# Kernel tuning notes

Measured on AMD Instinct MI355X. Metric: run time of the kernel, lower is better.

## Reference

```python
import jax, jax.numpy as jnp
import numpy as np

N_NODES = 50000
N_EDGES = 800000
F = 128
LN_EPS = 1e-5


def _sage_conv(h, src, dst, Wl, bl, Wr, n_nodes):
    # PyG SAGEConv (aggr='mean', root_weight=True):
    #   out_i = lin_l(mean_{j->i} h_j) + lin_r(h_i)
    msg = h[src]  # [E, F] irregular gather
    s = jax.ops.segment_sum(msg, dst, num_segments=n_nodes)  # [N, F]
    deg = jax.ops.segment_sum(jnp.ones((src.shape[0],), h.dtype), dst,
                              num_segments=n_nodes)  # [N]
    mean = s / jnp.maximum(deg, 1.0)[:, None]
    return mean @ Wl.T + bl + h @ Wr.T


def _graph_layernorm(h, w, b):
    # PyG LayerNorm mode='graph', batch=None: normalize over ALL entries,
    # eps added to std, then per-channel affine.
    m = h.mean()
    std = jnp.sqrt(jnp.mean((h - m) ** 2))
    return (h - m) / (std + LN_EPS) * w + b


def _prelu(h, w):
    # nn.PReLU(1): single shared slope
    return jnp.where(h >= 0, h, w * h)


def setup_inputs() -> dict:
    key = jax.random.key(0)
    ks = jax.random.split(key, 12)
    sc = 1.0 / np.sqrt(F)
    x = jax.random.normal(ks[0], (N_NODES, F), dtype=jnp.float32)
    edge_index = jax.random.randint(ks[1], (2, N_EDGES), 0, N_NODES, dtype=jnp.int64)
    return {
        "x": x,
        "edge_index": edge_index,
        "Wl0": jax.random.uniform(ks[2], (F, F), jnp.float32, -sc, sc),
        "bl0": jnp.zeros((F,), jnp.float32),
        "Wr0": jax.random.uniform(ks[3], (F, F), jnp.float32, -sc, sc),
        "ln_w0": jnp.ones((F,), jnp.float32),
        "ln_b0": jnp.zeros((F,), jnp.float32),
        "pw0": jnp.full((1,), 0.25, jnp.float32),
        "skipW0": jax.random.uniform(ks[4], (F, F), jnp.float32, -sc, sc),
        "Wl1": jax.random.uniform(ks[5], (F, F), jnp.float32, -sc, sc),
        "bl1": jnp.zeros((F,), jnp.float32),
        "Wr1": jax.random.uniform(ks[6], (F, F), jnp.float32, -sc, sc),
        "ln_w1": jnp.ones((F,), jnp.float32),
        "ln_b1": jnp.zeros((F,), jnp.float32),
        "pw1": jnp.full((1,), 0.25, jnp.float32),
    }


def reference(x, edge_index, Wl0, bl0, Wr0, ln_w0, ln_b0, pw0, skipW0,
              Wl1, bl1, Wr1, ln_w1, ln_b1, pw1):
    src, dst = edge_index[0], edge_index[1]
    n = x.shape[0]
    # layer 0: h = x
    h = _sage_conv(x, src, dst, Wl0, bl0, Wr0, n)
    h = _graph_layernorm(h, ln_w0, ln_b0)
    h1 = _prelu(h, pw0)
    # layer 1: h = skip(x) + h1
    h = x @ skipW0.T + h1
    h = _sage_conv(h, src, dst, Wl1, bl1, Wr1, n)
    h = _graph_layernorm(h, ln_w1, ln_b1)
    h = _prelu(h, pw1)
    return h
```

## Files before the change

kernel.cpp:

```cpp
#include <hip/hip_runtime.h>

#define LN_EPS 1e-5f
#define BUCKCAP 2048
#define PCHUNK 6656
#define PK 13

typedef short bf16x8 __attribute__((ext_vector_type(8)));
typedef float f32x4  __attribute__((ext_vector_type(4)));

static __device__ __forceinline__ float4 ld4(const float* p){ return *(const float4*)p; }
static __device__ __forceinline__ uint f2bf1(float f){
  uint u = __float_as_uint(f);
  return (u + 0x7fffu + ((u >> 16) & 1u)) >> 16;
}
static __device__ __forceinline__ float bf2f(uint lo16){ return __uint_as_float(lo16 << 16); }

__global__ __launch_bounds__(256) void prep_kernel(
    const float* __restrict__ x, ushort* __restrict__ x16, int nxb, int n8,
    const float* __restrict__ s0, const float* __restrict__ s1,
    const float* __restrict__ s2, const float* __restrict__ s3,
    const float* __restrict__ s4, ushort* __restrict__ wdst,
    double* __restrict__ stats, int* __restrict__ bcnt){
  int bid = blockIdx.x, tid = threadIdx.x;
  if (bid < nxb){
    int i = bid*256 + tid;
    if (i >= n8) return;
    float4 a = ld4(x + (size_t)i*8);
    float4 b = ld4(x + (size_t)i*8 + 4);
    uint4 o;
    o.x = f2bf1(a.x) | (f2bf1(a.y) << 16);
    o.y = f2bf1(a.z) | (f2bf1(a.w) << 16);
    o.z = f2bf1(b.x) | (f2bf1(b.y) << 16);
    o.w = f2bf1(b.z) | (f2bf1(b.w) << 16);
    *(uint4*)(x16 + (size_t)i*8) = o;
  } else if (bid < nxb + 40){
    int i = (bid - nxb)*256 + tid;
    int m = i >> 11;
    int o = (i & 2047) * 8;
    const float* s = (m == 0) ? s0 : (m == 1) ? s1 : (m == 2) ? s2 : (m == 3) ? s3 : s4;
    float4 a = ld4(s + o);
    float4 b = ld4(s + o + 4);
    uint4 v;
    v.x = f2bf1(a.x) | (f2bf1(a.y) << 16);
    v.y = f2bf1(a.z) | (f2bf1(a.w) << 16);
    v.z = f2bf1(b.x) | (f2bf1(b.y) << 16);
    v.w = f2bf1(b.z) | (f2bf1(b.w) << 16);
    *(uint4*)(wdst + (size_t)m*16384 + o) = v;
  } else {
    bcnt[tid] = 0; bcnt[tid + 256] = 0; bcnt[tid + 512] = 0; bcnt[tid + 768] = 0;
    if (tid < 4) stats[tid] = 0.0;
  }
}

__global__ __launch_bounds__(512) void partition_kernel(
    const int* __restrict__ ei, int E,
    int* __restrict__ bucket_count, uint* __restrict__ ebuf){
  __shared__ int hist[1024];
  __shared__ int base[1024];
  __shared__ int cur[1024];
  __shared__ int anyv;
  const int tid = threadIdx.x;
  const int lo = blockIdx.x * PCHUNK;
  const int hi = min(lo + PCHUNK, E);
  hist[tid] = 0; hist[tid + 512] = 0;
  if (tid == 0) anyv = 0;
  __syncthreads();
  int nz = 0;
  for (int i = tid; i < 1024; i += 512) nz |= (ei[2*i+1] != 0);
  if (nz) atomicOr(&anyv, 1);
  __syncthreads();
  const int fmt = anyv;

  uint pd[PK];
  #pragma unroll
  for (int k = 0; k < PK; k++){
    int e = lo + tid + k*512;
    uint v = 0xffffffffu;
    if (e < hi){
      int s, d;
      if (fmt){ s = ei[e]; d = ei[E + e]; }
      else    { s = ei[2*e]; d = ei[2*(E + e)]; }
      v = ((uint)d << 16) | (uint)s;
      atomicAdd(&hist[v >> 22], 1);
    }
    pd[k] = v;
  }
  __syncthreads();
  #pragma unroll
  for (int t0 = 0; t0 < 2; t0++){
    int t = tid + t0*512;
    int h = hist[t];
    base[t] = (h > 0) ? atomicAdd(&bucket_count[t], h) : 0;
    cur[t] = 0;
  }
  __syncthreads();
  #pragma unroll
  for (int k = 0; k < PK; k++){
    int e = lo + tid + k*512;
    if (e < hi){
      uint v = pd[k];
      int b = v >> 22;
      int pos = base[b] + atomicAdd(&cur[b], 1);
      if (pos < BUCKCAP) ebuf[(size_t)b*BUCKCAP + pos] = v;
    }
  }
}

template<int NMAT>
__global__ __launch_bounds__(512, 4) void agg_gemm(
    const ushort* __restrict__ h,
    const uint* __restrict__ ebuf, const int* __restrict__ bucket_count,
    const ushort* __restrict__ Wl, const ushort* __restrict__ Wr,
    const ushort* __restrict__ Wsk,
    const float* __restrict__ bias,
    ushort* __restrict__ tout, ushort* __restrict__ skout,
    int N, double* __restrict__ stats){
  __shared__ ushort ssrc[BUCKCAP];
  __shared__ int lcnt[64], lofs[64], lcur[64];
  __shared__ ushort Am[64][136];
  __shared__ double red[16];

  const int tid = threadIdx.x;
  const int b = blockIdx.x;
  const int n0 = b << 6;
  const uint* eb = ebuf + (size_t)b*BUCKCAP;
  const int cnt = min(bucket_count[b], BUCKCAP);

  if (tid < 64) lcnt[tid] = 0;
  __syncthreads();
  for (int e = tid; e < cnt; e += 512)
    atomicAdd(&lcnt[(eb[e] >> 16) & 63], 1);
  __syncthreads();
  if (tid < 64){
    int v = lcnt[tid];
    int s = v;
    #pragma unroll
    for (int off = 1; off < 64; off <<= 1){
      int u = __shfl_up(s, off);
      if (tid >= off) s += u;
    }
    lofs[tid] = s - v;
    lcur[tid] = s - v;
  }
  __syncthreads();
  for (int e = tid; e < cnt; e += 512){
    uint v = eb[e];
    int pos = atomicAdd(&lcur[(v >> 16) & 63], 1);
    ssrc[pos] = (ushort)(v & 0xffffu);
  }
  __syncthreads();

  const int wv = tid >> 6, lane = tid & 63;
  const uint* hp = (const uint*)h;
  #pragma unroll 1
  for (int i = 0; i < 8; i++){
    int j = wv*8 + i;
    int node = n0 + j;
    uint packed = 0;
    if (node < N){
      int start = lofs[j];
      int d = lcnt[j];
      float ax = 0.f, ay = 0.f;
      int e = 0;
      for (; e + 8 <= d; e += 8){
        uint v0 = hp[(size_t)ssrc[start+e+0]*64 + lane];
        uint v1 = hp[(size_t)ssrc[start+e+1]*64 + lane];
        uint v2 = hp[(size_t)ssrc[start+e+2]*64 + lane];
        uint v3 = hp[(size_t)ssrc[start+e+3]*64 + lane];
        uint v4 = hp[(size_t)ssrc[start+e+4]*64 + lane];
        uint v5 = hp[(size_t)ssrc[start+e+5]*64 + lane];
        uint v6 = hp[(size_t)ssrc[start+e+6]*64 + lane];
        uint v7 = hp[(size_t)ssrc[start+e+7]*64 + lane];
        ax += bf2f(v0 & 0xffffu) + bf2f(v1 & 0xffffu) + bf2f(v2 & 0xffffu) + bf2f(v3 & 0xffffu)
            + bf2f(v4 & 0xffffu) + bf2f(v5 & 0xffffu) + bf2f(v6 & 0xffffu) + bf2f(v7 & 0xffffu);
        ay += bf2f(v0 >> 16) + bf2f(v1 >> 16) + bf2f(v2 >> 16) + bf2f(v3 >> 16)
            + bf2f(v4 >> 16) + bf2f(v5 >> 16) + bf2f(v6 >> 16) + bf2f(v7 >> 16);
      }
      for (; e < d; e++){
        uint v = hp[(size_t)ssrc[start+e]*64 + lane];
        ax += bf2f(v & 0xffffu);
        ay += bf2f(v >> 16);
      }
      float inv = 1.f / fmaxf((float)d, 1.f);
      packed = f2bf1(ax*inv) | (f2bf1(ay*inv) << 16);
    }
    *(uint*)&Am[j][lane*2] = packed;
  }
  __syncthreads();

  const int wrow  = (wv & 3) * 16;
  const int chalf = (wv >> 2) * 64;
  const int lrow  = lane & 15;
  const int lk8   = (lane >> 4) * 8;

  f32x4 accT[4] = {};
  f32x4 accS[4] = {};

  #pragma unroll
  for (int ks = 0; ks < 4; ks++){
    const int kb = ks*32 + lk8;
    bf16x8 a1 = *(const bf16x8*)&Am[wrow + lrow][kb];
    int r = n0 + wrow + lrow; if (r > N-1) r = N-1;
    bf16x8 a2 = *(const bf16x8*)(h + (size_t)r*128 + kb);
    #pragma unroll
    for (int n = 0; n < 4; n++){
      const int c = chalf + n*16 + lrow;
      bf16x8 bl = *(const bf16x8*)(Wl + c*128 + kb);
      bf16x8 br = *(const bf16x8*)(Wr + c*128 + kb);
      accT[n] = __builtin_amdgcn_mfma_f32_16x16x32_bf16(a1, bl, accT[n], 0, 0, 0);
      accT[n] = __builtin_amdgcn_mfma_f32_16x16x32_bf16(a2, br, accT[n], 0, 0, 0);
      if (NMAT == 3){
        bf16x8 bs = *(const bf16x8*)(Wsk + c*128 + kb);
        accS[n] = __builtin_amdgcn_mfma_f32_16x16x32_bf16(a2, bs, accS[n], 0, 0, 0);
      }
    }
  }

  double ls1 = 0.0, ls2 = 0.0;
  const int rb = (lane >> 4) * 4;
  #pragma unroll
  for (int n = 0; n < 4; n++){
    const int col = chalf + n*16 + lrow;
    float bnv = bias[col];
    #pragma unroll
    for (int j = 0; j < 4; j++){
      int r = n0 + wrow + rb + j;
      if (r < N){
        float v = accT[n][j] + bnv;
        tout[(size_t)r*128 + col] = (ushort)f2bf1(v);
        ls1 += (double)v;
        ls2 += (double)v * (double)v;
        if (NMAT == 3)
          skout[(size_t)r*128 + col] = (ushort)f2bf1(accS[n][j]);
      }
    }
  }
  #pragma unroll
  for (int off = 32; off > 0; off >>= 1){
    ls1 += __shfl_down(ls1, off);
    ls2 += __shfl_down(ls2, off);
  }
  if (lane == 0){ red[wv*2] = ls1; red[wv*2+1] = ls2; }
  __syncthreads();
  if (tid == 0){
    double s1 = red[0]+red[2]+red[4]+red[6]+red[8]+red[10]+red[12]+red[14];
    atomicAdd(&stats[0], s1);
  }
  if (tid == 1){
    double s2 = red[1]+red[3]+red[5]+red[7]+red[9]+red[11]+red[13]+red[15];
    atomicAdd(&stats[1], s2);
  }
}

__global__ __launch_bounds__(256) void ln_skip_kernel(
    const ushort* __restrict__ t0, const ushort* __restrict__ sk,
    const double* __restrict__ stats,
    const float* __restrict__ lnw, const float* __restrict__ lnb,
    const float* __restrict__ pw, ushort* __restrict__ outb,
    int nu, double inv_cnt){
  double md = stats[0] * inv_cnt;
  double var = stats[1] * inv_cnt - md*md;
  float mean = (float)md;
  float rstd = 1.f / ((float)sqrt(fmax(var, 0.0)) + LN_EPS);
  float slope = pw[0];
  const uint* tp = (const uint*)t0;
  const uint* sp = (const uint*)sk;
  uint* op = (uint*)outb;
  for (int i = blockIdx.x*256 + threadIdx.x; i < nu; i += gridDim.x*256){
    int c = (i & 63) * 2;
    uint tv = tp[i], sv = sp[i];
    float l0 = (bf2f(tv & 0xffffu) - mean)*rstd*lnw[c]   + lnb[c];
    float l1 = (bf2f(tv >> 16)     - mean)*rstd*lnw[c+1] + lnb[c+1];
    l0 = (l0 >= 0.f) ? l0 : slope*l0;
    l1 = (l1 >= 0.f) ? l1 : slope*l1;
    float v0 = bf2f(sv & 0xffffu) + l0;
    float v1 = bf2f(sv >> 16)     + l1;
    op[i] = f2bf1(v0) | (f2bf1(v1) << 16);
  }
}

__global__ __launch_bounds__(256) void ln_out_kernel(
    const ushort* __restrict__ t1, const double* __restrict__ stats,
    const float* __restrict__ lnw, const float* __restrict__ lnb,
    const float* __restrict__ pw, float* __restrict__ out,
    int nu, double inv_cnt){
  double md = stats[0] * inv_cnt;
  double var = stats[1] * inv_cnt - md*md;
  float mean = (float)md;
  float rstd = 1.f / ((float)sqrt(fmax(var, 0.0)) + LN_EPS);
  float slope = pw[0];
  const uint* tp = (const uint*)t1;
  for (int i = blockIdx.x*256 + threadIdx.x; i < nu; i += gridDim.x*256){
    int c = (i & 63) * 2;
    uint tv = tp[i];
    float l0 = (bf2f(tv & 0xffffu) - mean)*rstd*lnw[c]   + lnb[c];
    float l1 = (bf2f(tv >> 16)     - mean)*rstd*lnw[c+1] + lnb[c+1];
    l0 = (l0 >= 0.f) ? l0 : slope*l0;
    l1 = (l1 >= 0.f) ? l1 : slope*l1;
    float2 v; v.x = l0; v.y = l1;
    *(float2*)(out + (size_t)i*2) = v;
  }
}

extern "C" void kernel_launch(void* const* d_in, const int* in_sizes, int n_in,
                              void* d_out, int out_size, void* d_ws, size_t ws_size,
                              hipStream_t stream){
  const float* x    = (const float*)d_in[0];
  const int*   ei   = (const int*)d_in[1];
  const float* Wl0  = (const float*)d_in[2];
  const float* bl0  = (const float*)d_in[3];
  const float* Wr0  = (const float*)d_in[4];
  const float* lnw0 = (const float*)d_in[5];
  const float* lnb0 = (const float*)d_in[6];
  const float* pw0  = (const float*)d_in[7];
  const float* skW  = (const float*)d_in[8];
  const float* Wl1  = (const float*)d_in[9];
  const float* bl1  = (const float*)d_in[10];
  const float* Wr1  = (const float*)d_in[11];
  const float* lnw1 = (const float*)d_in[12];
  const float* lnb1 = (const float*)d_in[13];
  const float* pw1  = (const float*)d_in[14];

  const int N = in_sizes[0] / 128;
  const int E = in_sizes[1] / 2;

  char* p = (char*)d_ws;
  auto carve = [&](size_t bytes)->char*{
    char* r = p;
    p += (bytes + 255) & ~(size_t)255;
    return r;
  };
  double* stats   = (double*)carve(4*sizeof(double));
  int*    bcnt    = (int*)carve((size_t)1024*4);
  uint*   ebuf    = (uint*)carve((size_t)1024*BUCKCAP*4);
  ushort* x16     = (ushort*)carve((size_t)N*128*2);
  ushort* tbuf16  = (ushort*)carve((size_t)N*128*2);
  ushort* skbuf16 = (ushort*)carve((size_t)N*128*2);
  ushort* hskip16 = (ushort*)carve((size_t)N*128*2);
  ushort* wbuf    = (ushort*)carve((size_t)5*16384*2);

  ushort* Wl0_16 = wbuf;
  ushort* Wr0_16 = wbuf + 16384;
  ushort* skW_16 = wbuf + 32768;
  ushort* Wl1_16 = wbuf + 49152;
  ushort* Wr1_16 = wbuf + 65536;

  const int n8  = N*16;
  const int nxb = (n8 + 255)/256;
  const int nbuck = (N + 63) >> 6;
  const int pb = (E + PCHUNK - 1) / PCHUNK;
  const double inv_cnt = 1.0 / ((double)N * 128.0);
  const int nu = N*64;

  prep_kernel<<<nxb + 40 + 1, 256, 0, stream>>>(x, x16, nxb, n8,
      Wl0, Wr0, skW, Wl1, Wr1, wbuf, stats, bcnt);
  partition_kernel<<<pb, 512, 0, stream>>>(ei, E, bcnt, ebuf);

  agg_gemm<3><<<nbuck, 512, 0, stream>>>(x16, ebuf, bcnt,
      Wl0_16, Wr0_16, skW_16, bl0, tbuf16, skbuf16, N, stats);
  ln_skip_kernel<<<2048, 256, 0, stream>>>(tbuf16, skbuf16, stats,
      lnw0, lnb0, pw0, hskip16, nu, inv_cnt);

  agg_gemm<2><<<nbuck, 512, 0, stream>>>(hskip16, ebuf, bcnt,
      Wl1_16, Wr1_16, nullptr, bl1, tbuf16, nullptr, N, stats + 2);
  ln_out_kernel<<<2048, 256, 0, stream>>>(tbuf16, stats + 2,
      lnw1, lnb1, pw1, (float*)d_out, nu, inv_cnt);
}
```

Baseline: 307.1 us.

## Split fused aggregate+GEMM into separate aggregation and GEMM kernels with finer buckets

Replaces the combined gather-mean-plus-MFMA kernel with two kernels. The first is a 32-node-bucket aggregation kernel that has two half-waves each gather a different edge with uint2 loads and then combines them through a shuffle. The second is a standalone GEMM over 128-row tiles that reads the materialized mean. Bucket count doubles (shift 21, cap 1024) to raise parallelism in the gather phase and let the GEMM use bigger tiles with better weight reuse. The cost is an extra N×128 bf16 write and read of the mean buffer and one more launch per layer. The lower per-bucket cap also raises the risk of silently dropping edges if a bucket overflows.

Result: faster. 267.6 us (-12.8%).

```diff
diff --git a/kernel.cpp b/kernel.cpp
--- a/kernel.cpp
+++ b/kernel.cpp
@@ -1,7 +1,8 @@
 #include <hip/hip_runtime.h>
 
 #define LN_EPS 1e-5f
-#define BUCKCAP 2048
+#define NBUCK_MAX 2048
+#define BUCKCAP 1024
 #define PCHUNK 6656
 #define PK 13
 
@@ -47,7 +48,8 @@
     v.w = f2bf1(b.z) | (f2bf1(b.w) << 16);
     *(uint4*)(wdst + (size_t)m*16384 + o) = v;
   } else {
-    bcnt[tid] = 0; bcnt[tid + 256] = 0; bcnt[tid + 512] = 0; bcnt[tid + 768] = 0;
+    #pragma unroll
+    for (int k = 0; k < 8; k++) bcnt[tid + k*256] = 0;
     if (tid < 4) stats[tid] = 0.0;
   }
 }
@@ -55,14 +57,15 @@
 __global__ __launch_bounds__(512) void partition_kernel(
     const int* __restrict__ ei, int E,
     int* __restrict__ bucket_count, uint* __restrict__ ebuf){
-  __shared__ int hist[1024];
-  __shared__ int base[1024];
-  __shared__ int cur[1024];
+  __shared__ int hist[NBUCK_MAX];
+  __shared__ int base[NBUCK_MAX];
+  __shared__ int cur[NBUCK_MAX];
   __shared__ int anyv;
   const int tid = threadIdx.x;
   const int lo = blockIdx.x * PCHUNK;
   const int hi = min(lo + PCHUNK, E);
-  hist[tid] = 0; hist[tid + 512] = 0;
+  #pragma unroll
+  for (int k = 0; k < 4; k++) hist[tid + k*512] = 0;
   if (tid == 0) anyv = 0;
   __syncthreads();
   int nz = 0;
@@ -81,13 +84,13 @@
       if (fmt){ s = ei[e]; d = ei[E + e]; }
       else    { s = ei[2*e]; d = ei[2*(E + e)]; }
       v = ((uint)d << 16) | (uint)s;
-      atomicAdd(&hist[v >> 22], 1);
+      atomicAdd(&hist[v >> 21], 1);
     }
     pd[k] = v;
   }
   __syncthreads();
   #pragma unroll
-  for (int t0 = 0; t0 < 2; t0++){
+  for (int t0 = 0; t0 < 4; t0++){
     int t = tid + t0*512;
     int h = hist[t];
     base[t] = (h > 0) ? atomicAdd(&bucket_count[t], h) : 0;
@@ -99,139 +102,174 @@
     int e = lo + tid + k*512;
     if (e < hi){
       uint v = pd[k];
-      int b = v >> 22;
+      int b = v >> 21;
       int pos = base[b] + atomicAdd(&cur[b], 1);
       if (pos < BUCKCAP) ebuf[(size_t)b*BUCKCAP + pos] = v;
     }
   }
 }
 
-template<int NMAT>
-__global__ __launch_bounds__(512, 4) void agg_gemm(
-    const ushort* __restrict__ h,
+__global__ __launch_bounds__(256) void bucket_aggregate(const ushort* __restrict__ h,
     const uint* __restrict__ ebuf, const int* __restrict__ bucket_count,
+    ushort* __restrict__ outmean, int N){
+  __shared__ ushort ssrc[BUCKCAP];
+  __shared__ int lcnt[32], lofs[32], lcur[32];
+  const int tid = threadIdx.x;
+  const int b = blockIdx.x;
+  const int n0 = b << 5;
+  const uint* eb = ebuf + (size_t)b*BUCKCAP;
+  const int cnt = min(bucket_count[b], BUCKCAP);
+
+  if (tid < 32) lcnt[tid] = 0;
+  __syncthreads();
+  for (int e = tid; e < cnt; e += 256)
+    atomicAdd(&lcnt[(eb[e] >> 16) & 31], 1);
+  __syncthreads();
+  if (tid < 32){
+    int v = lcnt[tid];
+    int s = v;
+    #pragma unroll
+    for (int off = 1; off < 32; off <<= 1){
+      int u = __shfl_up(s, off);
+      if (tid >= off) s += u;
+    }
+    lofs[tid] = s - v;
+    lcur[tid] = s - v;
+  }
+  __syncthreads();
+  for (int e = tid; e < cnt; e += 256){
+    uint v = eb[e];
+    int pos = atomicAdd(&lcur[(v >> 16) & 31], 1);
+    ssrc[pos] = (ushort)(v & 0xffffu);
+  }
+  __syncthreads();
+
+  const int wv = tid >> 6, lane = tid & 63;
+  const int half = lane >> 5;
+  const int col  = lane & 31;
+  const uint2* hp2 = (const uint2*)h;
+  uint2* op2 = (uint2*)outmean;
+  #pragma unroll 1
+  for (int i = 0; i < 8; i++){
+    int j = wv*8 + i;
+    int node = n0 + j;
+    if (node >= N) break;
+    int start = lofs[j];
+    int d = lcnt[j];
+    float f0 = 0.f, f1 = 0.f, f2 = 0.f, f3 = 0.f;
+    int e = 0;
+    for (; e + 8 <= d; e += 8){
+      int i0 = ssrc[start+e+0+half];
+      int i1 = ssrc[start+e+2+half];
+      int i2 = ssrc[start+e+4+half];
+      int i3 = ssrc[start+e+6+half];
+      uint2 v0 = hp2[(size_t)i0*32 + col];
+      uint2 v1 = hp2[(size_t)i1*32 + col];
+      uint2 v2 = hp2[(size_t)i2*32 + col];
+      uint2 v3 = hp2[(size_t)i3*32 + col];
+      f0 += bf2f(v0.x & 0xffffu) + bf2f(v1.x & 0xffffu) + bf2f(v2.x & 0xffffu) + bf2f(v3.x & 0xffffu);
+      f1 += bf2f(v0.x >> 16)     + bf2f(v1.x >> 16)     + bf2f(v2.x >> 16)     + bf2f(v3.x >> 16);
+      f2 += bf2f(v0.y & 0xffffu) + bf2f(v1.y & 0xffffu) + bf2f(v2.y & 0xffffu) + bf2f(v3.y & 0xffffu);
+      f3 += bf2f(v0.y >> 16)     + bf2f(v1.y >> 16)     + bf2f(v2.y >> 16)     + bf2f(v3.y >> 16);
+    }
+    for (; e + 2 <= d; e += 2){
+      int i0 = ssrc[start+e+half];
+      uint2 v = hp2[(size_t)i0*32 + col];
+      f0 += bf2f(v.x & 0xffffu);
+      f1 += bf2f(v.x >> 16);
+      f2 += bf2f(v.y & 0xffffu);
+      f3 += bf2f(v.y >> 16);
+    }
+    if (e < d && half == 0){
+      uint2 v = hp2[(size_t)ssrc[start+e]*32 + col];
+      f0 += bf2f(v.x & 0xffffu);
+      f1 += bf2f(v.x >> 16);
+      f2 += bf2f(v.y & 0xffffu);
+      f3 += bf2f(v.y >> 16);
+    }
+    f0 += __shfl_xor(f0, 32);
+    f1 += __shfl_xor(f1, 32);
+    f2 += __shfl_xor(f2, 32);
+    f3 += __shfl_xor(f3, 32);
+    if (half == 0){
+      float inv = 1.f / fmaxf((float)d, 1.f);
+      uint2 o;
+      o.x = f2bf1(f0*inv) | (f2bf1(f1*inv) << 16);
+      o.y = f2bf1(f2*inv) | (f2bf1(f3*inv) << 16);
+      op2[(size_t)node*32 + col] = o;
+    }
+  }
+}
+
+template<int SKIP>
+__global__ __launch_bounds__(256) void gemm_fused(
+    const ushort* __restrict__ A1, const ushort* __restrict__ A2,
     const ushort* __restrict__ Wl, const ushort* __restrict__ Wr,
     const ushort* __restrict__ Wsk,
     const float* __restrict__ bias,
     ushort* __restrict__ tout, ushort* __restrict__ skout,
     int N, double* __restrict__ stats){
-  __shared__ ushort ssrc[BUCKCAP];
-  __shared__ int lcnt[64], lofs[64], lcur[64];
-  __shared__ ushort Am[64][136];
-  __shared__ double red[16];
-
-  const int tid = threadIdx.x;
-  const int b = blockIdx.x;
-  const int n0 = b << 6;
-  const uint* eb = ebuf + (size_t)b*BUCKCAP;
-  const int cnt = min(bucket_count[b], BUCKCAP);
-
-  if (tid < 64) lcnt[tid] = 0;
-  __syncthreads();
-  for (int e = tid; e < cnt; e += 512)
-    atomicAdd(&lcnt[(eb[e] >> 16) & 63], 1);
-  __syncthreads();
-  if (tid < 64){
-    int v = lcnt[tid];
-    int s = v;
+  const int tid  = threadIdx.x;
+  const int lane = tid & 63;
+  const int wv   = tid >> 6;
+  const int r0   = blockIdx.x*128 + wv*32;
+  const int lrow = lane & 15;
+  const int lk   = (lane >> 4) * 8;
+
+  f32x4 accT[2][8] = {};
+  f32x4 accS[2][8] = {};
+
+  #pragma unroll
+  for (int ks = 0; ks < 4; ks++){
+    const int kb = ks*32 + lk;
+    bf16x8 a1[2], a2[2];
     #pragma unroll
-    for (int off = 1; off < 64; off <<= 1){
-      int u = __shfl_up(s, off);
-      if (tid >= off) s += u;
-    }
-    lofs[tid] = s - v;
-    lcur[tid] = s - v;
-  }
-  __syncthreads();
-  for (int e = tid; e < cnt; e += 512){
-    uint v = eb[e];
-    int pos = atomicAdd(&lcur[(v >> 16) & 63], 1);
-    ssrc[pos] = (ushort)(v & 0xffffu);
-  }
-  __syncthreads();
-
-  const int wv = tid >> 6, lane = tid & 63;
-  const uint* hp = (const uint*)h;
-  #pragma unroll 1
-  for (int i = 0; i < 8; i++){
-    int j = wv*8 + i;
-    int node = n0 + j;
-    uint packed = 0;
-    if (node < N){
-      int start = lofs[j];
-      int d = lcnt[j];
-      float ax = 0.f, ay = 0.f;
-      int e = 0;
-      for (; e + 8 <= d; e += 8){
-        uint v0 = hp[(size_t)ssrc[start+e+0]*64 + lane];
-        uint v1 = hp[(size_t)ssrc[start+e+1]*64 + lane];
-        uint v2 = hp[(size_t)ssrc[start+e+2]*64 + lane];
-        uint v3 = hp[(size_t)ssrc[start+e+3]*64 + lane];
-        uint v4 = hp[(size_t)ssrc[start+e+4]*64 + lane];
-        uint v5 = hp[(size_t)ssrc[start+e+5]*64 + lane];
-        uint v6 = hp[(size_t)ssrc[start+e+6]*64 + lane];
-        uint v7 = hp[(size_t)ssrc[start+e+7]*64 + lane];
-        ax += bf2f(v0 & 0xffffu) + bf2f(v1 & 0xffffu) + bf2f(v2 & 0xffffu) + bf2f(v3 & 0xffffu)
-            + bf2f(v4 & 0xffffu) + bf2f(v5 & 0xffffu) + bf2f(v6 & 0xffffu) + bf2f(v7 & 0xffffu);
-        ay += bf2f(v0 >> 16) + bf2f(v1 >> 16) + bf2f(v2 >> 16) + bf2f(v3 >> 16)
-            + bf2f(v4 >> 16) + bf2f(v5 >> 16) + bf2f(v6 >> 16) + bf2f(v7 >> 16);
-      }
-      for (; e < d; e++){
-        uint v = hp[(size_t)ssrc[start+e]*64 + lane];
-        ax += bf2f(v & 0xffffu);
-        ay += bf2f(v >> 16);
-      }
-      float inv = 1.f / fmaxf((float)d, 1.f);
-      packed = f2bf1(ax*inv) | (f2bf1(ay*inv) << 16);
-    }
-    *(uint*)&Am[j][lane*2] = packed;
-  }
-  __syncthreads();
-
-  const int wrow  = (wv & 3) * 16;
-  const int chalf = (wv >> 2) * 64;
-  const int lrow  = lane & 15;
-  const int lk8   = (lane >> 4) * 8;
-
-  f32x4 accT[4] = {};
-  f32x4 accS[4] = {};
-
-  #pragma unroll
-  for (int ks = 0; ks < 4; ks++){
-    const int kb = ks*32 + lk8;
-    bf16x8 a1 = *(const bf16x8*)&Am[wrow + lrow][kb];
-    int r = n0 + wrow + lrow; if (r > N-1) r = N-1;
-    bf16x8 a2 = *(const bf16x8*)(h + (size_t)r*128 + kb);
+    for (int m = 0; m < 2; m++){
+      int r = r0 + m*16 + lrow;
+      if (r > N-1) r = N-1;
+      a1[m] = *(const bf16x8*)(A1 + (size_t)r*128 + kb);
+      a2[m] = *(const bf16x8*)(A2 + (size_t)r*128 + kb);
+    }
     #pragma unroll
-    for (int n = 0; n < 4; n++){
-      const int c = chalf + n*16 + lrow;
+    for (int n = 0; n < 8; n++){
+      const int c = n*16 + lrow;
       bf16x8 bl = *(const bf16x8*)(Wl + c*128 + kb);
       bf16x8 br = *(const bf16x8*)(Wr + c*128 + kb);
-      accT[n] = __builtin_amdgcn_mfma_f32_16x16x32_bf16(a1, bl, accT[n], 0, 0, 0);
-      accT[n] = __builtin_amdgcn_mfma_f32_16x16x32_bf16(a2, br, accT[n], 0, 0, 0);
-      if (NMAT == 3){
+      #pragma unroll
+      for (int m = 0; m < 2; m++){
+        accT[m][n] = __builtin_amdgcn_mfma_f32_16x16x32_bf16(a1[m], bl, accT[m][n], 0, 0, 0);
+        accT[m][n] = __builtin_amdgcn_mfma_f32_16x16x32_bf16(a2[m], br, accT[m][n], 0, 0, 0);
+      }
+      if (SKIP){
         bf16x8 bs = *(const bf16x8*)(Wsk + c*128 + kb);
-        accS[n] = __builtin_amdgcn_mfma_f32_16x16x32_bf16(a2, bs, accS[n], 0, 0, 0);
+        #pragma unroll
+        for (int m = 0; m < 2; m++)
+          accS[m][n] = __builtin_amdgcn_mfma_f32_16x16x32_bf16(a2[m], bs, accS[m][n], 0, 0, 0);
       }
     }
   }
+
+  float bn[8];
+  #pragma unroll
+  for (int n = 0; n < 8; n++) bn[n] = bias[n*16 + lrow];
 
   double ls1 = 0.0, ls2 = 0.0;
   const int rb = (lane >> 4) * 4;
   #pragma unroll
-  for (int n = 0; n < 4; n++){
-    const int col = chalf + n*16 + lrow;
-    float bnv = bias[col];
+  for (int m = 0; m < 2; m++){
     #pragma unroll
     for (int j = 0; j < 4; j++){
-      int r = n0 + wrow + rb + j;
+      int r = r0 + m*16 + rb + j;
       if (r < N){
-        float v = accT[n][j] + bnv;
-        tout[(size_t)r*128 + col] = (ushort)f2bf1(v);
-        ls1 += (double)v;
-        ls2 += (double)v * (double)v;
-        if (NMAT == 3)
-          skout[(size_t)r*128 + col] = (ushort)f2bf1(accS[n][j]);
+        #pragma unroll
+        for (int n = 0; n < 8; n++){
+          float v = accT[m][n][j] + bn[n];
+          tout[(size_t)r*128 + n*16 + lrow] = (ushort)f2bf1(v);
+          ls1 += (double)v;
+          ls2 += (double)v * (double)v;
+          if (SKIP)
+            skout[(size_t)r*128 + n*16 + lrow] = (ushort)f2bf1(accS[m][n][j]);
+        }
       }
     }
   }
@@ -240,16 +278,11 @@
     ls1 += __shfl_down(ls1, off);
     ls2 += __shfl_down(ls2, off);
   }
+  __shared__ double red[8];
   if (lane == 0){ red[wv*2] = ls1; red[wv*2+1] = ls2; }
   __syncthreads();
-  if (tid == 0){
-    double s1 = red[0]+red[2]+red[4]+red[6]+red[8]+red[10]+red[12]+red[14];
-    atomicAdd(&stats[0], s1);
-  }
-  if (tid == 1){
-    double s2 = red[1]+red[3]+red[5]+red[7]+red[9]+red[11]+red[13]+red[15];
-    atomicAdd(&stats[1], s2);
-  }
+  if (tid == 0) atomicAdd(&stats[0], red[0]+red[2]+red[4]+red[6]);
+  if (tid == 1) atomicAdd(&stats[1], red[1]+red[3]+red[5]+red[7]);
 }
 
 __global__ __launch_bounds__(256) void ln_skip_kernel(
@@ -331,9 +364,10 @@
     return r;
   };
   double* stats   = (double*)carve(4*sizeof(double));
-  int*    bcnt    = (int*)carve((size_t)1024*4);
-  uint*   ebuf    = (uint*)carve((size_t)1024*BUCKCAP*4);
+  int*    bcnt    = (int*)carve((size_t)NBUCK_MAX*4);
+  uint*   ebuf    = (uint*)carve((size_t)NBUCK_MAX*BUCKCAP*4);
   ushort* x16     = (ushort*)carve((size_t)N*128*2);
+  ushort* mean16  = (ushort*)carve((size_t)N*128*2);
   ushort* tbuf16  = (ushort*)carve((size_t)N*128*2);
   ushort* skbuf16 = (ushort*)carve((size_t)N*128*2);
   ushort* hskip16 = (ushort*)carve((size_t)N*128*2);
@@ -347,8 +381,9 @@
 
   const int n8  = N*16;
   const int nxb = (n8 + 255)/256;
-  const int nbuck = (N + 63) >> 6;
+  const int nbuck = (N + 31) >> 5;
   const int pb = (E + PCHUNK - 1) / PCHUNK;
+  const int gb = (N + 127)/128;
   const double inv_cnt = 1.0 / ((double)N * 128.0);
   const int nu = N*64;
 
@@ -356,13 +391,15 @@
       Wl0, Wr0, skW, Wl1, Wr1, wbuf, stats, bcnt);
   partition_kernel<<<pb, 512, 0, stream>>>(ei, E, bcnt, ebuf);
 
-  agg_gemm<3><<<nbuck, 512, 0, stream>>>(x16, ebuf, bcnt,
-      Wl0_16, Wr0_16, skW_16, bl0, tbuf16, skbuf16, N, stats);
+  bucket_aggregate<<<nbuck, 256, 0, stream>>>(x16, ebuf, bcnt, mean16, N);
+  gemm_fused<1><<<gb, 256, 0, stream>>>(mean16, x16, Wl0_16, Wr0_16, skW_16,
+      bl0, tbuf16, skbuf16, N, stats);
   ln_skip_kernel<<<2048, 256, 0, stream>>>(tbuf16, skbuf16, stats,
       lnw0, lnb0, pw0, hskip16, nu, inv_cnt);
 
-  agg_gemm<2><<<nbuck, 512, 0, stream>>>(hskip16, ebuf, bcnt,
-      Wl1_16, Wr1_16, nullptr, bl1, tbuf16, nullptr, N, stats + 2);
+  bucket_aggregate<<<nbuck, 256, 0, stream>>>(hskip16, ebuf, bcnt, mean16, N);
+  gemm_fused<0><<<gb, 256, 0, stream>>>(mean16, hskip16, Wl1_16, Wr1_16, nullptr,
+      bl1, tbuf16, nullptr, N, stats + 2);
   ln_out_kernel<<<2048, 256, 0, stream>>>(tbuf16, stats + 2,
       lnw1, lnb1, pw1, (float*)d_out, nu, inv_cnt);
 }
```
